# Kernel tuning notes

Hardware: AMD Instinct MI355X
Metric: run time of the kernel (lower is better)

The kernel has to match this reference:

```python
import jax, jax.numpy as jnp
import numpy as np
import math

WH, WW = 8, 8          # window size
NH = 16                # num heads
C = 512                # dim
N = WH * WW            # tokens per window


def _rel_tables():
    # continuous relative coords table, shape [(2WH-1)*(2WW-1), 2]
    ch = jnp.arange(-(WH - 1), WH, dtype=jnp.float32)
    cw = jnp.arange(-(WW - 1), WW, dtype=jnp.float32)
    t = jnp.stack(jnp.meshgrid(ch, cw, indexing='ij'), axis=-1)  # [2WH-1, 2WW-1, 2]
    t = t / jnp.array([WH - 1, WW - 1], dtype=jnp.float32)
    t = t * 8.0
    t = jnp.sign(t) * jnp.log2(jnp.abs(t) + 1.0) / np.float32(math.log2(8))
    t = t.reshape(-1, 2)
    # relative position index, shape [N, N], values in [0, (2WH-1)*(2WW-1))
    coords = np.stack(np.meshgrid(np.arange(WH), np.arange(WW), indexing='ij'))  # [2,WH,WW]
    cf = coords.reshape(2, -1)
    rel = (cf[:, :, None] - cf[:, None, :]).transpose(1, 2, 0).astype(np.int64)
    rel[..., 0] += WH - 1
    rel[..., 1] += WW - 1
    rel[..., 0] *= 2 * WW - 1
    idx = rel.sum(-1)
    return t, jnp.asarray(idx)


def setup_inputs() -> dict:
    key = jax.random.key(0)
    ks = jax.random.split(key, 12)
    B_ = 4096
    num_win = 256
    s = lambda k, shape, sc: jax.random.normal(k, shape, dtype=jnp.float32) * sc
    return {
        'x': s(ks[0], (B_, N, C), 1.0),
        'mask': s(ks[1], (num_win, N, N), 1.0),
        'qkv_w': s(ks[2], (3 * C, C), 0.02),
        'q_bias': s(ks[3], (C,), 0.02),
        'v_bias': s(ks[4], (C,), 0.02),
        'logit_scale': jnp.full((NH, 1, 1), math.log(10.0), dtype=jnp.float32),
        'cpb_w1': s(ks[5], (512, 2), 0.1),
        'cpb_b1': s(ks[6], (512,), 0.1),
        'cpb_w2': s(ks[7], (NH, 512), 0.1),
        'proj_w': s(ks[8], (C, C), 0.02),
        'proj_b': s(ks[9], (C,), 0.02),
    }


def reference(x, mask, qkv_w, q_bias, v_bias, logit_scale, cpb_w1, cpb_b1, cpb_w2, proj_w, proj_b):
    B_, n, c = x.shape
    hd = c // NH
    coords_table, rel_idx = _rel_tables()

    # qkv projection with (q_bias, 0, v_bias) bias
    qkv_bias = jnp.concatenate([q_bias, jnp.zeros_like(q_bias), v_bias])
    qkv = x @ qkv_w.T + qkv_bias                       # [B_, N, 3C]
    qkv = qkv.reshape(B_, n, 3, NH, hd).transpose(2, 0, 3, 1, 4)
    q, k, v = qkv[0], qkv[1], qkv[2]                   # [B_, NH, N, hd]

    # cosine attention
    qn = q / jnp.linalg.norm(q, axis=-1, keepdims=True)
    kn = k / jnp.linalg.norm(k, axis=-1, keepdims=True)
    attn = jnp.einsum('bhnd,bhmd->bhnm', qn, kn)       # [B_, NH, N, N]
    scale = jnp.exp(jnp.minimum(logit_scale, math.log(1.0 / 0.01)))
    attn = attn * scale                                 # broadcast [NH,1,1]

    # CPB-MLP relative position bias
    hidden = jax.nn.relu(coords_table @ cpb_w1.T + cpb_b1)   # [T, 512]
    table = hidden @ cpb_w2.T                                # [T, NH]
    bias = table[rel_idx.reshape(-1)].reshape(n, n, NH)      # [N, N, NH]
    bias = 16.0 * jax.nn.sigmoid(bias.transpose(2, 0, 1))    # [NH, N, N]
    attn = attn + bias[None]

    # shifted-window mask add
    num_win = mask.shape[0]
    attn = attn.reshape(B_ // num_win, num_win, NH, n, n) + mask[None, :, None]
    attn = attn.reshape(B_, NH, n, n)
    attn = jax.nn.softmax(attn, axis=-1)

    out = jnp.einsum('bhnm,bhmd->bhnd', attn, v)       # [B_, NH, N, hd]
    out = out.transpose(0, 2, 1, 3).reshape(B_, n, c)
    out = out @ proj_w.T + proj_b
    return out
```

## Files before the change

### kernel.cpp

```cpp
#include <hip/hip_runtime.h>
#include <math.h>

typedef __bf16 bf16_t;
typedef __bf16 bf16x8 __attribute__((ext_vector_type(8)));
typedef __bf16 bf16x4 __attribute__((ext_vector_type(4)));
typedef float  f32x4  __attribute__((ext_vector_type(4)));

__device__ __forceinline__ void gll16(const void* g, void* l) {
    __builtin_amdgcn_global_load_lds((const __attribute__((address_space(1))) void*)g,
                                     (__attribute__((address_space(3))) void*)l, 16, 0, 0);
}

__global__ void cvt_bf16(const float* __restrict__ in, bf16_t* __restrict__ out, long n) {
    long i = ((long)blockIdx.x * blockDim.x + threadIdx.x) * 4;
    long stride = (long)gridDim.x * blockDim.x * 4;
    for (; i < n; i += stride) {
        float4 v = *(const float4*)(in + i);
        bf16x4 o;
        o[0] = (bf16_t)v.x; o[1] = (bf16_t)v.y; o[2] = (bf16_t)v.z; o[3] = (bf16_t)v.w;
        *(bf16x4*)(out + i) = o;
    }
}

__global__ void build_qkv_bias(const float* __restrict__ qb, const float* __restrict__ vb,
                               float* __restrict__ out) {
    int i = blockIdx.x * blockDim.x + threadIdx.x;
    float v = 0.f;
    if (i < 512) v = qb[i];
    else if (i >= 1024) v = vb[i - 1024];
    out[i] = v;
}

__global__ void cpb_tab(const float* __restrict__ w1, const float* __restrict__ b1,
                        const float* __restrict__ w2, float* __restrict__ tab) {
    __shared__ float hid[512];
    int e = blockIdx.x;
    int ci = e / 15, cj = e % 15;
    int t = threadIdx.x;
    float a0 = (float)(ci - 7) * (8.0f / 7.0f);
    float a1 = (float)(cj - 7) * (8.0f / 7.0f);
    float s0 = (a0 > 0.f) ? 1.f : ((a0 < 0.f) ? -1.f : 0.f);
    float s1 = (a1 > 0.f) ? 1.f : ((a1 < 0.f) ? -1.f : 0.f);
    float t0 = s0 * log2f(fabsf(a0) + 1.f) * (1.f / 3.f);
    float t1 = s1 * log2f(fabsf(a1) + 1.f) * (1.f / 3.f);
    float hv = t0 * w1[t * 2] + t1 * w1[t * 2 + 1] + b1[t];
    hid[t] = hv > 0.f ? hv : 0.f;
    __syncthreads();
    int g = t >> 5, l = t & 31;
    float s = 0.f;
    for (int q = l; q < 512; q += 32) s += hid[q] * w2[g * 512 + q];
    s += __shfl_xor(s, 1);  s += __shfl_xor(s, 2);  s += __shfl_xor(s, 4);
    s += __shfl_xor(s, 8);  s += __shfl_xor(s, 16);
    if (l == 0) tab[e * 16 + g] = s;
}

__global__ void cpb_expand(const float* __restrict__ tab, float* __restrict__ biasx) {
    int idx = blockIdx.x * blockDim.x + threadIdx.x;
    int h = idx >> 12;
    int rem = idx & 4095;
    int t1 = rem >> 6, t2 = rem & 63;
    int dh = (t1 >> 3) - (t2 >> 3) + 7;
    int dw = (t1 & 7) - (t2 & 7) + 7;
    float v = tab[(dh * 15 + dw) * 16 + h];
    biasx[idx] = 16.0f / (1.0f + __expf(-v));
}

template <int OUT_BF16>
__global__ __launch_bounds__(256) void gemm_bt(
    const bf16_t* __restrict__ A, const bf16_t* __restrict__ B,
    const float* __restrict__ bias, void* __restrict__ Cout,
    int M, int N, int K) {
    __shared__ __attribute__((aligned(16))) bf16_t As[128 * 32];
    __shared__ __attribute__((aligned(16))) bf16_t Bs[128 * 32];
    const int tid = threadIdx.x;
    const int wv = tid >> 6;
    const int ln = tid & 63;
    const int quad = ln >> 4;
    const int l15 = ln & 15;
    const int bn = blockIdx.x;
    const int bm = blockIdx.y;
    const long row0 = (long)bm * 128;
    const int col0 = bn * 128;
    const int wm = (wv >> 1) * 64;
    const int wn = (wv & 1) * 64;

    f32x4 acc[4][4] = {};

    const int srow = wv * 16 + (ln >> 2);
    const int skc = (ln & 3) * 8;

    for (int k0 = 0; k0 < K; k0 += 32) {
        __syncthreads();
        const bf16_t* ga0 = A + (row0 + srow) * (long)K + k0 + skc;
        const bf16_t* ga1 = A + (row0 + 64 + srow) * (long)K + k0 + skc;
        const bf16_t* gb0 = B + (long)(col0 + srow) * K + k0 + skc;
        const bf16_t* gb1 = B + (long)(col0 + 64 + srow) * K + k0 + skc;
        char* lA = (char*)As + wv * 1024;
        char* lB = (char*)Bs + wv * 1024;
        gll16(ga0, lA);
        gll16(ga1, lA + 4096);
        gll16(gb0, lB);
        gll16(gb1, lB + 4096);
        __syncthreads();
        bf16x8 af[4], bfr[4];
#pragma unroll
        for (int i = 0; i < 4; ++i)
            af[i] = *(const bf16x8*)&As[(wm + i * 16 + l15) * 32 + quad * 8];
#pragma unroll
        for (int j = 0; j < 4; ++j)
            bfr[j] = *(const bf16x8*)&Bs[(wn + j * 16 + l15) * 32 + quad * 8];
#pragma unroll
        for (int i = 0; i < 4; ++i)
#pragma unroll
            for (int j = 0; j < 4; ++j)
                acc[i][j] = __builtin_amdgcn_mfma_f32_16x16x32_bf16(af[i], bfr[j], acc[i][j], 0, 0, 0);
    }
#pragma unroll
    for (int i = 0; i < 4; ++i) {
        const long rb = row0 + wm + i * 16 + quad * 4;
#pragma unroll
        for (int j = 0; j < 4; ++j) {
            const int c = col0 + wn + j * 16 + l15;
            const float bv = bias[c];
#pragma unroll
            for (int r = 0; r < 4; ++r) {
                float v = acc[i][j][r] + bv;
                if (OUT_BF16)
                    ((bf16_t*)Cout)[(rb + r) * (long)N + c] = (bf16_t)v;
                else
                    ((float*)Cout)[(rb + r) * (long)N + c] = v;
            }
        }
    }
}

__device__ __forceinline__ void load_norm_row(const bf16_t* g, bf16_t* lds_row) {
    bf16x8 t[4];
#pragma unroll
    for (int i = 0; i < 4; ++i) t[i] = *(const bf16x8*)(g + i * 8);
    float f[32];
    float ss = 0.f;
#pragma unroll
    for (int i = 0; i < 4; ++i)
#pragma unroll
        for (int e = 0; e < 8; ++e) {
            float v = (float)t[i][e];
            f[i * 8 + e] = v;
            ss += v * v;
        }
    float inv = rsqrtf(ss);
#pragma unroll
    for (int i = 0; i < 4; ++i) {
        bf16x8 o;
#pragma unroll
        for (int e = 0; e < 8; ++e) o[e] = (bf16_t)(f[i * 8 + e] * inv);
        *(bf16x8*)(lds_row + i * 8) = o;
    }
}

__global__ __launch_bounds__(64) void attn64(
    const bf16_t* __restrict__ qkv,
    const float* __restrict__ mask,
    const float* __restrict__ biasx,
    const float* __restrict__ lsc,
    bf16_t* __restrict__ outa) {
    __shared__ __attribute__((aligned(16))) bf16_t qs[64 * 32];
    __shared__ __attribute__((aligned(16))) bf16_t ks[64 * 32];
    __shared__ __attribute__((aligned(16))) bf16_t vt[32 * 64];
    __shared__ __attribute__((aligned(16))) bf16_t ps[64 * 64];
    const int b = blockIdx.x;
    const int h = blockIdx.y;
    const int ln = threadIdx.x;
    const int quad = ln >> 4, l15 = ln & 15;
    const long rowbase = (long)b * 64 * 1536;
    const bf16_t* qrow = qkv + rowbase + ln * 1536 + h * 32;

    load_norm_row(qrow, &qs[ln * 32]);
    load_norm_row(qrow + 512, &ks[ln * 32]);
    {
        const bf16_t* vr = qrow + 1024;
        bf16x8 t[4];
#pragma unroll
        for (int i = 0; i < 4; ++i) t[i] = *(const bf16x8*)(vr + i * 8);
#pragma unroll
        for (int i = 0; i < 4; ++i)
#pragma unroll
            for (int e = 0; e < 8; ++e) vt[(i * 8 + e) * 64 + ln] = t[i][e];
    }
    __syncthreads();

    f32x4 sa[4][4] = {};
    {
        bf16x8 af[4], bfr[4];
#pragma unroll
        for (int i = 0; i < 4; ++i)
            af[i] = *(const bf16x8*)&qs[(i * 16 + l15) * 32 + quad * 8];
#pragma unroll
        for (int j = 0; j < 4; ++j)
            bfr[j] = *(const bf16x8*)&ks[(j * 16 + l15) * 32 + quad * 8];
#pragma unroll
        for (int i = 0; i < 4; ++i)
#pragma unroll
            for (int j = 0; j < 4; ++j)
                sa[i][j] = __builtin_amdgcn_mfma_f32_16x16x32_bf16(af[i], bfr[j], sa[i][j], 0, 0, 0);
    }

    const float scale = __expf(fminf(lsc[h], 4.60517019f));
    const float* mrow = mask + (long)(b & 255) * 4096;
    const float* brow = biasx + h * 4096;

#pragma unroll
    for (int i = 0; i < 4; ++i)
#pragma unroll
        for (int j = 0; j < 4; ++j)
#pragma unroll
            for (int r = 0; r < 4; ++r) {
                int rr = i * 16 + quad * 4 + r;
                int cc = j * 16 + l15;
                sa[i][j][r] = sa[i][j][r] * scale + brow[rr * 64 + cc] + mrow[rr * 64 + cc];
            }

    float rmax[4][4], rsum[4][4];
#pragma unroll
    for (int i = 0; i < 4; ++i)
#pragma unroll
        for (int r = 0; r < 4; ++r) {
            float m = sa[i][0][r];
#pragma unroll
            for (int j = 1; j < 4; ++j) m = fmaxf(m, sa[i][j][r]);
            m = fmaxf(m, __shfl_xor(m, 1));
            m = fmaxf(m, __shfl_xor(m, 2));
            m = fmaxf(m, __shfl_xor(m, 4));
            m = fmaxf(m, __shfl_xor(m, 8));
            rmax[i][r] = m;
        }
#pragma unroll
    for (int i = 0; i < 4; ++i)
#pragma unroll
        for (int r = 0; r < 4; ++r) {
            float s = 0.f;
#pragma unroll
            for (int j = 0; j < 4; ++j) {
                float e = __expf(sa[i][j][r] - rmax[i][r]);
                sa[i][j][r] = e;
                s += e;
            }
            s += __shfl_xor(s, 1);
            s += __shfl_xor(s, 2);
            s += __shfl_xor(s, 4);
            s += __shfl_xor(s, 8);
            rsum[i][r] = s;
        }
#pragma unroll
    for (int i = 0; i < 4; ++i)
#pragma unroll
        for (int j = 0; j < 4; ++j)
#pragma unroll
            for (int r = 0; r < 4; ++r) {
                float p = sa[i][j][r] / rsum[i][r];
                ps[(i * 16 + quad * 4 + r) * 64 + j * 16 + l15] = (bf16_t)p;
            }
    __syncthreads();

    f32x4 oa[4][2] = {};
#pragma unroll
    for (int kst = 0; kst < 2; ++kst) {
        bf16x8 pf[4], vf[2];
#pragma unroll
        for (int i = 0; i < 4; ++i)
            pf[i] = *(const bf16x8*)&ps[(i * 16 + l15) * 64 + kst * 32 + quad * 8];
#pragma unroll
        for (int n2 = 0; n2 < 2; ++n2)
            vf[n2] = *(const bf16x8*)&vt[(n2 * 16 + l15) * 64 + kst * 32 + quad * 8];
#pragma unroll
        for (int i = 0; i < 4; ++i)
#pragma unroll
            for (int n2 = 0; n2 < 2; ++n2)
                oa[i][n2] = __builtin_amdgcn_mfma_f32_16x16x32_bf16(pf[i], vf[n2], oa[i][n2], 0, 0, 0);
    }
#pragma unroll
    for (int i = 0; i < 4; ++i)
#pragma unroll
        for (int n2 = 0; n2 < 2; ++n2)
#pragma unroll
            for (int r = 0; r < 4; ++r) {
                long row = (long)b * 64 + i * 16 + quad * 4 + r;
                int col = h * 32 + n2 * 16 + l15;
                outa[row * 512 + col] = (bf16_t)oa[i][n2][r];
            }
}

extern "C" void kernel_launch(void* const* d_in, const int* in_sizes, int n_in,
                              void* d_out, int out_size, void* d_ws, size_t ws_size,
                              hipStream_t stream) {
    const float* x           = (const float*)d_in[0];
    const float* mask        = (const float*)d_in[1];
    const float* qkv_w       = (const float*)d_in[2];
    const float* q_bias      = (const float*)d_in[3];
    const float* v_bias      = (const float*)d_in[4];
    const float* logit_scale = (const float*)d_in[5];
    const float* cpb_w1      = (const float*)d_in[6];
    const float* cpb_b1      = (const float*)d_in[7];
    const float* cpb_w2      = (const float*)d_in[8];
    const float* proj_w      = (const float*)d_in[9];
    const float* proj_b      = (const float*)d_in[10];
    float* out = (float*)d_out;

    char* w = (char*)d_ws;
    bf16_t* qkvb = (bf16_t*)w;          w += (size_t)402653184 * 2;
    bf16_t* xb   = (bf16_t*)w;          w += (size_t)134217728 * 2;
    bf16_t* attn_o = xb;
    bf16_t* qkvw_b = (bf16_t*)w;        w += (size_t)786432 * 2;
    bf16_t* projw_b = (bf16_t*)w;       w += (size_t)262144 * 2;
    float* biasx = (float*)w;           w += (size_t)65536 * 4;
    float* qkv_bias = (float*)w;        w += (size_t)1536 * 4;
    float* tab = (float*)w;             w += (size_t)3600 * 4;

    cvt_bf16<<<8192, 256, 0, stream>>>(x, xb, 134217728L);
    cvt_bf16<<<768, 256, 0, stream>>>(qkv_w, qkvw_b, 786432L);
    cvt_bf16<<<256, 256, 0, stream>>>(proj_w, projw_b, 262144L);
    build_qkv_bias<<<6, 256, 0, stream>>>(q_bias, v_bias, qkv_bias);
    cpb_tab<<<225, 512, 0, stream>>>(cpb_w1, cpb_b1, cpb_w2, tab);
    cpb_expand<<<64, 1024, 0, stream>>>(tab, biasx);

    dim3 g1(12, 2048);
    gemm_bt<1><<<g1, 256, 0, stream>>>(xb, qkvw_b, qkv_bias, qkvb, 262144, 1536, 512);

    dim3 ga(4096, 16);
    attn64<<<ga, 64, 0, stream>>>(qkvb, mask, biasx, logit_scale, attn_o);

    dim3 g2(4, 2048);
    gemm_bt<0><<<g2, 256, 0, stream>>>(attn_o, projw_b, proj_b, out, 262144, 512, 512);
}
```

Before: 2.310 ms.

## Replace GEMM with 256x256 double-buffered, swizzled-LDS pipelined MFMA kernel

Replaces the 128x128 single-buffered GEMM with a 256x256-tile, 512-thread kernel. It double-buffers K=64 slices in 128KB of LDS and interleaves global-to-LDS staging with quarter-tile MFMA phases, using explicit barriers, waitcnts and setprio. The kernel XOR-swizzles LDS columns to avoid bank conflicts and remaps block IDs for L2 locality. The aim is higher MFMA utilization and more data reuse per tile, at the cost of heavy LDS use that limits occupancy and fragile manual synchronization.

Result: faster. 2.041 ms (-11.7%).

```diff
diff --git a/kernel.cpp b/kernel.cpp
--- a/kernel.cpp
+++ b/kernel.cpp
@@ -10,6 +10,10 @@
     __builtin_amdgcn_global_load_lds((const __attribute__((address_space(1))) void*)g,
                                      (__attribute__((address_space(3))) void*)l, 16, 0, 0);
 }
+
+#define BAR()   do { __builtin_amdgcn_s_barrier(); asm volatile("" ::: "memory"); } while (0)
+#define LGKM0() asm volatile("s_waitcnt lgkmcnt(0)" ::: "memory")
+#define VMW(n)  asm volatile("s_waitcnt vmcnt(" #n ")" ::: "memory")
 
 __global__ void cvt_bf16(const float* __restrict__ in, bf16_t* __restrict__ out, long n) {
     long i = ((long)blockIdx.x * blockDim.x + threadIdx.x) * 4;
@@ -65,66 +69,122 @@
     biasx[idx] = 16.0f / (1.0f + __expf(-v));
 }
 
+#define MMAQ(qm, qn, bfr)                                                          \
+  do {                                                                             \
+    __builtin_amdgcn_s_setprio(1);                                                 \
+    _Pragma("unroll") for (int i_ = 0; i_ < 4; ++i_)                               \
+      _Pragma("unroll") for (int j_ = 0; j_ < 2; ++j_)                             \
+        _Pragma("unroll") for (int kk_ = 0; kk_ < 2; ++kk_)                        \
+          acc[(qm)*4 + i_][(qn)*2 + j_] = __builtin_amdgcn_mfma_f32_16x16x32_bf16( \
+              a[i_][kk_], bfr[j_][kk_], acc[(qm)*4 + i_][(qn)*2 + j_], 0, 0, 0);   \
+    __builtin_amdgcn_s_setprio(0);                                                 \
+  } while (0)
+
 template <int OUT_BF16>
-__global__ __launch_bounds__(256) void gemm_bt(
+__global__ __launch_bounds__(512, 2) void gemm256(
     const bf16_t* __restrict__ A, const bf16_t* __restrict__ B,
     const float* __restrict__ bias, void* __restrict__ Cout,
-    int M, int N, int K) {
-    __shared__ __attribute__((aligned(16))) bf16_t As[128 * 32];
-    __shared__ __attribute__((aligned(16))) bf16_t Bs[128 * 32];
+    int N, int K, int nTN) {
+    __shared__ __attribute__((aligned(16))) char lds[131072];
     const int tid = threadIdx.x;
-    const int wv = tid >> 6;
-    const int ln = tid & 63;
-    const int quad = ln >> 4;
-    const int l15 = ln & 15;
-    const int bn = blockIdx.x;
-    const int bm = blockIdx.y;
-    const long row0 = (long)bm * 128;
-    const int col0 = bn * 128;
-    const int wm = (wv >> 1) * 64;
-    const int wn = (wv & 1) * 64;
-
-    f32x4 acc[4][4] = {};
-
-    const int srow = wv * 16 + (ln >> 2);
-    const int skc = (ln & 3) * 8;
-
-    for (int k0 = 0; k0 < K; k0 += 32) {
-        __syncthreads();
-        const bf16_t* ga0 = A + (row0 + srow) * (long)K + k0 + skc;
-        const bf16_t* ga1 = A + (row0 + 64 + srow) * (long)K + k0 + skc;
-        const bf16_t* gb0 = B + (long)(col0 + srow) * K + k0 + skc;
-        const bf16_t* gb1 = B + (long)(col0 + 64 + srow) * K + k0 + skc;
-        char* lA = (char*)As + wv * 1024;
-        char* lB = (char*)Bs + wv * 1024;
-        gll16(ga0, lA);
-        gll16(ga1, lA + 4096);
-        gll16(gb0, lB);
-        gll16(gb1, lB + 4096);
-        __syncthreads();
-        bf16x8 af[4], bfr[4];
-#pragma unroll
-        for (int i = 0; i < 4; ++i)
-            af[i] = *(const bf16x8*)&As[(wm + i * 16 + l15) * 32 + quad * 8];
-#pragma unroll
-        for (int j = 0; j < 4; ++j)
-            bfr[j] = *(const bf16x8*)&Bs[(wn + j * 16 + l15) * 32 + quad * 8];
-#pragma unroll
-        for (int i = 0; i < 4; ++i)
-#pragma unroll
-            for (int j = 0; j < 4; ++j)
-                acc[i][j] = __builtin_amdgcn_mfma_f32_16x16x32_bf16(af[i], bfr[j], acc[i][j], 0, 0, 0);
-    }
+    const int wid = tid >> 6;
+    const int ln  = tid & 63;
+    const int quad = ln >> 4, l15 = ln & 15;
+    const int wm2 = wid >> 2, wn4 = wid & 3;
+
+    const int nwg = gridDim.x;
+    const int bid = blockIdx.x;
+    const int swz = (bid & 7) * (nwg >> 3) + (bid >> 3);
+    const int bm = swz / nTN, bn = swz % nTN;
+    const long arow0 = (long)bm * 256;
+    const int  bcol0 = bn * 256;
+    const int  nt = K >> 6;
+
+    const int srow = wid * 16 + (ln >> 3);
+    const int scol = ((ln & 7) ^ (ln >> 3)) * 8;
+    const bf16_t* gA = A + (arow0 + srow) * (long)K + scol;
+    const bf16_t* gB = B + ((long)bcol0 + srow) * (long)K + scol;
+    const long rK8 = (long)K * 8;
+    const int ldsw = wid * 2048;
+
+    const int cb0 = (quad * 16) ^ ((l15 & 7) << 4);
+
+    f32x4 acc[8][4] = {};
+    bf16x8 a[4][2], b0[2][2], b1[2][2];
+
+    auto stageA = [&](int v, int hi) {
+        char* d = &lds[((v & 1) << 16) + (hi << 14) + ldsw];
+        const bf16_t* s = gA + (long)(hi * 128) * K + v * 64;
+        gll16(s, d);
+        gll16(s + rK8, d + 1024);
+    };
+    auto stageB = [&](int v, int hi) {
+        char* d = &lds[((v & 1) << 16) + 32768 + (hi << 14) + ldsw];
+        const bf16_t* s = gB + (long)(hi * 128) * K + v * 64;
+        gll16(s, d);
+        gll16(s + rK8, d + 1024);
+    };
+    auto ldA = [&](int buf, int qm) {
+#pragma unroll
+        for (int i = 0; i < 4; ++i) {
+            const char* p = &lds[(buf << 16) + (wm2 * 128 + qm * 64 + i * 16 + l15) * 128];
+            a[i][0] = *(const bf16x8*)(p + cb0);
+            a[i][1] = *(const bf16x8*)(p + (cb0 ^ 64));
+        }
+    };
+    auto ldB = [&](bf16x8 (&bf)[2][2], int buf, int qn) {
+#pragma unroll
+        for (int j = 0; j < 2; ++j) {
+            const char* p = &lds[(buf << 16) + 32768 + (wn4 * 64 + qn * 32 + j * 16 + l15) * 128];
+            bf[j][0] = *(const bf16x8*)(p + cb0);
+            bf[j][1] = *(const bf16x8*)(p + (cb0 ^ 64));
+        }
+    };
+
+    stageA(0, 0); stageA(0, 1); stageB(0, 0); stageB(0, 1);
+    if (nt > 1) { stageB(1, 0); stageB(1, 1); VMW(4); }
+    else        { VMW(0); }
+    BAR();
+
+    for (int u = 0; u < nt; ++u) {
+        const int buf = u & 1;
+        ldA(buf, 0); ldB(b0, buf, 0);
+        if (u + 1 < nt) stageA(u + 1, 0);
+        BAR(); LGKM0();
+        MMAQ(0, 0, b0);
+        BAR();
+        ldB(b1, buf, 1);
+        if (u + 1 < nt) stageA(u + 1, 1);
+        BAR(); LGKM0();
+        MMAQ(0, 1, b1);
+        BAR();
+        ldA(buf, 1);
+        if (u + 2 < nt) stageB(u + 2, 0);
+        BAR(); LGKM0();
+        MMAQ(1, 1, b1);
+        BAR();
+        if (u + 2 < nt) stageB(u + 2, 1);
+        BAR();
+        MMAQ(1, 0, b0);
+        if (u + 2 < nt) { VMW(4); } else { VMW(0); }
+        BAR();
+    }
+
+#pragma unroll
+    for (int qm = 0; qm < 2; ++qm)
 #pragma unroll
     for (int i = 0; i < 4; ++i) {
-        const long rb = row0 + wm + i * 16 + quad * 4;
-#pragma unroll
-        for (int j = 0; j < 4; ++j) {
-            const int c = col0 + wn + j * 16 + l15;
+        const long rb = arow0 + wm2 * 128 + qm * 64 + i * 16 + quad * 4;
+#pragma unroll
+        for (int qn = 0; qn < 2; ++qn)
+#pragma unroll
+        for (int j = 0; j < 2; ++j) {
+            const int c = bcol0 + wn4 * 64 + qn * 32 + j * 16 + l15;
             const float bv = bias[c];
+            const f32x4 v4 = acc[qm * 4 + i][qn * 2 + j];
 #pragma unroll
             for (int r = 0; r < 4; ++r) {
-                float v = acc[i][j][r] + bv;
+                float v = v4[r] + bv;
                 if (OUT_BF16)
                     ((bf16_t*)Cout)[(rb + r) * (long)N + c] = (bf16_t)v;
                 else
@@ -323,12 +383,10 @@
     cpb_tab<<<225, 512, 0, stream>>>(cpb_w1, cpb_b1, cpb_w2, tab);
     cpb_expand<<<64, 1024, 0, stream>>>(tab, biasx);
 
-    dim3 g1(12, 2048);
-    gemm_bt<1><<<g1, 256, 0, stream>>>(xb, qkvw_b, qkv_bias, qkvb, 262144, 1536, 512);
+    gemm256<1><<<dim3(6144), 512, 0, stream>>>(xb, qkvw_b, qkv_bias, qkvb, 1536, 512, 6);
 
     dim3 ga(4096, 16);
     attn64<<<ga, 64, 0, stream>>>(qkvb, mask, biasx, logit_scale, attn_o);
 
-    dim3 g2(4, 2048);
-    gemm_bt<0><<<g2, 256, 0, stream>>>(attn_o, projw_b, proj_b, out, 262144, 512, 512);
-}
+    gemm256<0><<<dim3(2048), 512, 0, stream>>>(attn_o, projw_b, proj_b, out, 512, 512, 2);
+}
```
